# Kernel tuning notes

Hardware: AMD Instinct MI355X
Metric: run time of the kernel (lower is better)

Reference implementation:

```python
import jax, jax.numpy as jnp
import numpy as np

N = 1048576   # samples
C = 64        # classes (Y unique targets)
S = 8         # subgroups


def setup_inputs() -> dict:
    key = jax.random.key(0)
    k1, k2, k3 = jax.random.split(key, 3)
    logits = jax.random.normal(k1, (N, C), dtype=jnp.float32)
    targets = jax.random.randint(k2, (N,), 0, C, dtype=jnp.int64)
    subgroup_inf = jax.random.randint(k3, (N,), 0, S, dtype=jnp.int64)
    return {"logits": logits, "targets": targets, "subgroup_inf": subgroup_inf}


def reference(logits, targets, subgroup_inf):
    # per-sample cross-entropy (loss_fn with reduction='none')
    logp = jax.nn.log_softmax(logits, axis=-1)                       # [N, C]
    per_sample = -jnp.take_along_axis(logp, targets[:, None], axis=-1)[:, 0]  # [N]

    # composite (target, subgroup) key -> group counts via one scatter-add
    key_ids = targets * S + subgroup_inf                              # [N]
    counts = jax.ops.segment_sum(jnp.ones_like(per_sample), key_ids,
                                 num_segments=C * S)                  # [C*S]
    # every sample's own group has count >= 1, so no div-by-zero
    weighted = per_sample / counts[key_ids]
    return jnp.sum(weighted)
```

## Files before the change

### kernel.cpp

```cpp
#include <hip/hip_runtime.h>


#define NKEYS 512

__global__ __launch_bounds__(256)
void orl_count_kernel(const int* __restrict__ targets,
                      const int* __restrict__ subg,
                      unsigned int* __restrict__ counts, int n) {
    __shared__ unsigned int hist[NKEYS];
    for (int i = threadIdx.x; i < NKEYS; i += blockDim.x) hist[i] = 0u;
    __syncthreads();
    int stride = gridDim.x * blockDim.x;
    for (int i = blockIdx.x * blockDim.x + threadIdx.x; i < n; i += stride) {
        int key = targets[i] * 8 + subg[i];
        atomicAdd(&hist[key], 1u);
    }
    __syncthreads();
    for (int i = threadIdx.x; i < NKEYS; i += blockDim.x) {
        unsigned int v = hist[i];
        if (v) atomicAdd(&counts[i], v);
    }
}

__global__ __launch_bounds__(256)
void orl_loss_kernel(const float* __restrict__ logits,
                     const int* __restrict__ targets,
                     const int* __restrict__ subg,
                     const unsigned int* __restrict__ counts,
                     float* __restrict__ out, int n) {
    const int row = blockIdx.x * blockDim.x + threadIdx.x;
    float weighted = 0.0f;
    if (row < n) {
        const float4* rp = (const float4*)(logits + (size_t)row * 64);
        float sum = 0.0f;
        #pragma unroll
        for (int j = 0; j < 16; ++j) {
            float4 v = rp[j];
            sum += __expf(v.x) + __expf(v.y) + __expf(v.z) + __expf(v.w);
        }
        const int t = targets[row];
        const float xt = logits[(size_t)row * 64 + t];
        const float lse = __logf(sum);
        const float per_sample = lse - xt;
        const int key = t * 8 + subg[row];
        const float cnt = (float)counts[key];
        weighted = per_sample * __builtin_amdgcn_rcpf(cnt);
    }
    #pragma unroll
    for (int off = 32; off > 0; off >>= 1)
        weighted += __shfl_down(weighted, off, 64);
    __shared__ float wsum[4];
    const int lane = threadIdx.x & 63;
    const int wid  = threadIdx.x >> 6;
    if (lane == 0) wsum[wid] = weighted;
    __syncthreads();
    if (threadIdx.x == 0) {
        atomicAdd(out, wsum[0] + wsum[1] + wsum[2] + wsum[3]);
    }
}

extern "C" void kernel_launch(void* const* d_in, const int* in_sizes, int n_in,
                              void* d_out, int out_size, void* d_ws, size_t ws_size,
                              hipStream_t stream) {
    const float* logits  = (const float*)d_in[0];
    const int*   targets = (const int*)d_in[1];
    const int*   subg    = (const int*)d_in[2];
    const int n = in_sizes[1];
    float* out = (float*)d_out;
    unsigned int* counts = (unsigned int*)d_ws;

    hipMemsetAsync(counts, 0, NKEYS * sizeof(unsigned int), stream);
    hipMemsetAsync(out, 0, sizeof(float), stream);

    orl_count_kernel<<<1024, 256, 0, stream>>>(targets, subg, counts, n);

    const int blocks = (n + 255) / 256;
    orl_loss_kernel<<<blocks, 256, 0, stream>>>(logits, targets, subg, counts, out, n);
}
```

Before: 387.0 us.

## Fuse counting and loss via per-group loss sums divided at the end

Rewrites the sum as the sum over groups of (group loss sum / group count), which lets one pass accumulate per-key loss sums and counts in shared memory and a tiny final kernel do the divisions. Logit rows are now read by 16-lane groups with coalesced float4 loads and a shuffle reduction, replacing the one-row-per-thread strided reads. The count pre-pass and second read of targets/subgroups go away. In exchange it adds shared-memory float atomics that may contend, and the summation order changes.

Result: faster. 376.0 us (-2.8%).

```diff
diff --git a/kernel.cpp b/kernel.cpp
--- a/kernel.cpp
+++ b/kernel.cpp
@@ -3,59 +3,88 @@
 
 #define NKEYS 512
 
+__device__ __forceinline__ float pick4(float4 v, int j) {
+    float r = v.x;
+    r = (j == 1) ? v.y : r;
+    r = (j == 2) ? v.z : r;
+    r = (j == 3) ? v.w : r;
+    return r;
+}
+
 __global__ __launch_bounds__(256)
-void orl_count_kernel(const int* __restrict__ targets,
+void orl_fused_kernel(const float* __restrict__ logits,
+                      const int* __restrict__ targets,
                       const int* __restrict__ subg,
-                      unsigned int* __restrict__ counts, int n) {
-    __shared__ unsigned int hist[NKEYS];
-    for (int i = threadIdx.x; i < NKEYS; i += blockDim.x) hist[i] = 0u;
+                      float* __restrict__ gsum,
+                      unsigned int* __restrict__ gcnt,
+                      int n) {
+    __shared__ float        lsum[NKEYS];
+    __shared__ unsigned int lcnt[NKEYS];
+    for (int i = threadIdx.x; i < NKEYS; i += 256) { lsum[i] = 0.0f; lcnt[i] = 0u; }
     __syncthreads();
-    int stride = gridDim.x * blockDim.x;
-    for (int i = blockIdx.x * blockDim.x + threadIdx.x; i < n; i += stride) {
-        int key = targets[i] * 8 + subg[i];
-        atomicAdd(&hist[key], 1u);
+
+    const int lane = threadIdx.x & 63;
+    const int q    = lane & 15;
+    const int g    = lane >> 4;
+    const int wave = (blockIdx.x << 2) | (threadIdx.x >> 6);
+    const int nwaves = gridDim.x << 2;
+
+    for (int base = wave * 8; base < n; base += nwaves * 8) {
+        const int rowA = base + g;
+        const int rowB = base + 4 + g;
+        const float4 vA = *(const float4*)(logits + (size_t)rowA * 64 + q * 4);
+        const float4 vB = *(const float4*)(logits + (size_t)rowB * 64 + q * 4);
+        const int tA = targets[rowA];
+        const int tB = targets[rowB];
+
+        float sA = __expf(vA.x) + __expf(vA.y) + __expf(vA.z) + __expf(vA.w);
+        float sB = __expf(vB.x) + __expf(vB.y) + __expf(vB.z) + __expf(vB.w);
+        #pragma unroll
+        for (int m = 1; m < 16; m <<= 1) {
+            sA += __shfl_xor(sA, m, 16);
+            sB += __shfl_xor(sB, m, 16);
+        }
+        if ((tA >> 2) == q) {
+            const float ps = __logf(sA) - pick4(vA, tA & 3);
+            const int key = tA * 8 + subg[rowA];
+            atomicAdd(&lsum[key], ps);
+            atomicAdd(&lcnt[key], 1u);
+        }
+        if ((tB >> 2) == q) {
+            const float ps = __logf(sB) - pick4(vB, tB & 3);
+            const int key = tB * 8 + subg[rowB];
+            atomicAdd(&lsum[key], ps);
+            atomicAdd(&lcnt[key], 1u);
+        }
     }
+
     __syncthreads();
-    for (int i = threadIdx.x; i < NKEYS; i += blockDim.x) {
-        unsigned int v = hist[i];
-        if (v) atomicAdd(&counts[i], v);
+    for (int i = threadIdx.x; i < NKEYS; i += 256) {
+        const unsigned int c = lcnt[i];
+        if (c) {
+            atomicAdd(&gsum[i], lsum[i]);
+            atomicAdd(&gcnt[i], c);
+        }
     }
 }
 
-__global__ __launch_bounds__(256)
-void orl_loss_kernel(const float* __restrict__ logits,
-                     const int* __restrict__ targets,
-                     const int* __restrict__ subg,
-                     const unsigned int* __restrict__ counts,
-                     float* __restrict__ out, int n) {
-    const int row = blockIdx.x * blockDim.x + threadIdx.x;
-    float weighted = 0.0f;
-    if (row < n) {
-        const float4* rp = (const float4*)(logits + (size_t)row * 64);
-        float sum = 0.0f;
+__global__ __launch_bounds__(512)
+void orl_final_kernel(const float* __restrict__ gsum,
+                      const unsigned int* __restrict__ gcnt,
+                      float* __restrict__ out) {
+    const int k = threadIdx.x;
+    const unsigned int c = gcnt[k];
+    float v = c ? gsum[k] / (float)c : 0.0f;
+    #pragma unroll
+    for (int m = 32; m > 0; m >>= 1) v += __shfl_down(v, m, 64);
+    __shared__ float wsum[8];
+    if ((k & 63) == 0) wsum[k >> 6] = v;
+    __syncthreads();
+    if (k == 0) {
+        float t = 0.0f;
         #pragma unroll
-        for (int j = 0; j < 16; ++j) {
-            float4 v = rp[j];
-            sum += __expf(v.x) + __expf(v.y) + __expf(v.z) + __expf(v.w);
-        }
-        const int t = targets[row];
-        const float xt = logits[(size_t)row * 64 + t];
-        const float lse = __logf(sum);
-        const float per_sample = lse - xt;
-        const int key = t * 8 + subg[row];
-        const float cnt = (float)counts[key];
-        weighted = per_sample * __builtin_amdgcn_rcpf(cnt);
-    }
-    #pragma unroll
-    for (int off = 32; off > 0; off >>= 1)
-        weighted += __shfl_down(weighted, off, 64);
-    __shared__ float wsum[4];
-    const int lane = threadIdx.x & 63;
-    const int wid  = threadIdx.x >> 6;
-    if (lane == 0) wsum[wid] = weighted;
-    __syncthreads();
-    if (threadIdx.x == 0) {
-        atomicAdd(out, wsum[0] + wsum[1] + wsum[2] + wsum[3]);
+        for (int w = 0; w < 8; ++w) t += wsum[w];
+        out[0] = t;
     }
 }
 
@@ -67,13 +96,12 @@
     const int*   subg    = (const int*)d_in[2];
     const int n = in_sizes[1];
     float* out = (float*)d_out;
-    unsigned int* counts = (unsigned int*)d_ws;
 
-    hipMemsetAsync(counts, 0, NKEYS * sizeof(unsigned int), stream);
-    hipMemsetAsync(out, 0, sizeof(float), stream);
+    float*        gsum = (float*)d_ws;
+    unsigned int* gcnt = (unsigned int*)((char*)d_ws + NKEYS * sizeof(float));
 
-    orl_count_kernel<<<1024, 256, 0, stream>>>(targets, subg, counts, n);
+    hipMemsetAsync(d_ws, 0, NKEYS * (sizeof(float) + sizeof(unsigned int)), stream);
 
-    const int blocks = (n + 255) / 256;
-    orl_loss_kernel<<<blocks, 256, 0, stream>>>(logits, targets, subg, counts, out, n);
+    orl_fused_kernel<<<1024, 256, 0, stream>>>(logits, targets, subg, gsum, gcnt, n);
+    orl_final_kernel<<<1, 512, 0, stream>>>(gsum, gcnt, out);
 }
```
